# Kernel optimization log

Hardware: AMD Instinct MI355X
Metric: run time of the kernel (lower is better)

Reference implementation:

```python
import jax, jax.numpy as jnp
import numpy as np

BS, V, J = 256, 10475, 55
NSHAPE, NEXP = 300, 50

# SMPLX kinematic tree (fixed model constant)
PARENTS = np.array([
    -1, 0, 0, 0, 1, 2, 3, 4, 5, 6, 7, 8, 9, 9, 9, 12, 13, 14, 16, 17, 18, 19,
    15, 15, 15,
    20, 25, 26, 20, 28, 29, 20, 31, 32, 20, 34, 35, 20, 37, 38,
    21, 40, 41, 21, 43, 44, 21, 46, 47, 21, 49, 50, 21, 52, 53], dtype=np.int64)


def batch_rodrigues(rvec):
    # rvec: [N,3] axis-angle -> [N,3,3] rotation matrices
    angle = jnp.linalg.norm(rvec + 1e-8, axis=-1, keepdims=True)  # [N,1]
    axis = rvec / angle
    x, y, z = axis[..., 0], axis[..., 1], axis[..., 2]
    zr = jnp.zeros_like(x)
    K = jnp.stack([zr, -z, y, z, zr, -x, -y, x, zr], axis=-1).reshape(-1, 3, 3)
    s = jnp.sin(angle)[..., None]
    c = jnp.cos(angle)[..., None]
    I = jnp.eye(3, dtype=rvec.dtype)
    return I + s * K + (1.0 - c) * (K @ K)


def setup_inputs():
    key = jax.random.key(0)
    ks = jax.random.split(key, 9)
    pose = 0.2 * jax.random.normal(ks[0], (BS, 53, 3), jnp.float32)
    shape = jax.random.normal(ks[1], (BS, 10), jnp.float32)
    expression = jax.random.normal(ks[2], (BS, NEXP), jnp.float32)
    global_orient = 0.2 * jax.random.normal(ks[3], (1, 3), jnp.float32)
    v_template = jax.random.normal(ks[4], (V, 3), jnp.float32)
    shapedirs = 0.01 * jax.random.normal(ks[5], (V, 3, NSHAPE + NEXP), jnp.float32)
    posedirs = 0.01 * jax.random.normal(ks[6], (486, V * 3), jnp.float32)
    J_regressor = jax.random.uniform(ks[7], (J, V), jnp.float32)
    J_regressor = J_regressor / jnp.sum(J_regressor, axis=1, keepdims=True)
    lbs_weights = jax.random.uniform(ks[8], (V, J), jnp.float32)
    lbs_weights = lbs_weights / jnp.sum(lbs_weights, axis=1, keepdims=True)
    return {"pose": pose, "shape": shape, "expression": expression,
            "global_orient": global_orient, "v_template": v_template,
            "shapedirs": shapedirs, "posedirs": posedirs,
            "J_regressor": J_regressor, "lbs_weights": lbs_weights}


def lbs(betas, rot_mats, v_template, shapedirs, posedirs, J_regressor, lbs_weights):
    bs = betas.shape[0]
    dt = betas.dtype
    # shape blendshapes
    v_shaped = v_template[None] + jnp.einsum('bl,vcl->bvc', betas, shapedirs)
    # rest-pose joints
    joints = jnp.einsum('jv,bvc->bjc', J_regressor, v_shaped)  # [b,J,3]
    # pose blendshapes
    I3 = jnp.eye(3, dtype=dt)
    pose_feature = (rot_mats[:, 1:] - I3).reshape(bs, -1)  # [b,(J-1)*9]
    v_posed = v_shaped + jnp.einsum('bp,pn->bn', pose_feature, posedirs).reshape(bs, V, 3)
    # forward kinematics along the tree
    rel_joints = jnp.concatenate(
        [joints[:, :1], joints[:, 1:] - joints[:, PARENTS[1:]]], axis=1)
    top = jnp.concatenate([rot_mats, rel_joints[..., None]], axis=-1)  # [b,J,3,4]
    bot = jnp.broadcast_to(jnp.array([0, 0, 0, 1], dtype=dt), (bs, J, 1, 4))
    T_local = jnp.concatenate([top, bot], axis=-2)  # [b,J,4,4]
    A_list = [T_local[:, 0]]
    for j in range(1, J):  # fixed 55-joint chain
        A_list.append(A_list[int(PARENTS[j])] @ T_local[:, j])
    A = jnp.stack(A_list, axis=1)  # [b,J,4,4]
    posed_joints = A[..., :3, 3]
    # subtract rest-pose contribution
    corr = jnp.einsum('bjmn,bjn->bjm', A[..., :3, :3], joints)
    A_rel = A.at[..., :3, 3].add(-corr)
    # vertex skinning
    T = jnp.einsum('vj,bjmn->bvmn', lbs_weights, A_rel)  # [b,V,4,4]
    verts = jnp.einsum('bvmn,bvn->bvm', T[..., :3, :3], v_posed) + T[..., :3, 3]
    return verts, posed_joints


def reference(pose, shape, expression, global_orient, v_template, shapedirs,
              posedirs, J_regressor, lbs_weights):
    bs = pose.shape[0]
    dt = pose.dtype
    go = jnp.broadcast_to(global_orient[:, None, :], (bs, 1, 3))
    eyes = jnp.zeros((bs, 2, 3), dtype=dt)  # leye/reye fixed at zero
    # order: global, body(21), jaw, leye, reye, lhand(15), rhand(15) -> 55
    full_pose = jnp.concatenate(
        [go, pose[:, 1:22], pose[:, 52:53], eyes, pose[:, 22:37], pose[:, 37:52]],
        axis=1)
    betas = jnp.concatenate(
        [shape, jnp.zeros((bs, NSHAPE - shape.shape[1]), dtype=dt), expression],
        axis=1)  # [b,350]
    rot_mats = batch_rodrigues(full_pose.reshape(-1, 3)).reshape(bs, J, 3, 3)
    verts, joints = lbs(betas, rot_mats, v_template, shapedirs, posedirs,
                        J_regressor, lbs_weights)
    return verts, joints
```

## Files before the change

kernel.cpp:

```cpp
#include <hip/hip_runtime.h>
#include <math.h>

#define BS 256
#define V 10475
#define NJ 55
#define R3 31425
#define NP 486
#define LB 60
#define KP 576
#define VK 10496
#define JOFF 8044800
#define DSP 66

typedef __attribute__((ext_vector_type(8))) short short8;
typedef __attribute__((ext_vector_type(4))) float float4_;

__device__ const int PARENTS_d[NJ] = {
  -1, 0, 0, 0, 1, 2, 3, 4, 5, 6, 7, 8, 9, 9, 9, 12, 13, 14, 16, 17, 18, 19,
  15, 15, 15, 20, 25, 26, 20, 28, 29, 20, 31, 32, 20, 34, 35, 20, 37, 38,
  21, 40, 41, 21, 43, 44, 21, 46, 47, 21, 49, 50, 21, 52, 53
};

__device__ __forceinline__ unsigned short f2b(float f) {
  unsigned int u = __float_as_uint(f);
  unsigned int r = (u + 0x7FFFu + ((u >> 16) & 1u)) >> 16;
  return (unsigned short)r;
}

__global__ __launch_bounds__(256) void k_pose(
    const float* __restrict__ pose, const float* __restrict__ shp,
    const float* __restrict__ expr, const float* __restrict__ go,
    float* __restrict__ rot_ws, unsigned short* __restrict__ Ftr,
    float* __restrict__ betas_T) {
  int b = threadIdx.x;
  int j = blockIdx.x;
  if (j == NJ) {
    #pragma unroll
    for (int l = 0; l < 10; ++l) {
      float v = shp[b * 10 + l];
      betas_T[l * BS + b] = v;
      Ftr[(size_t)b * KP + NP + l] = f2b(v);
    }
    #pragma unroll
    for (int l = 0; l < 50; ++l) {
      float v = expr[b * 50 + l];
      betas_T[(10 + l) * BS + b] = v;
      Ftr[(size_t)b * KP + NP + 10 + l] = f2b(v);
    }
    #pragma unroll
    for (int l = NP + LB; l < KP; ++l) Ftr[(size_t)b * KP + l] = 0;
    return;
  }
  float rx, ry, rz;
  if (j == 0) { rx = go[0]; ry = go[1]; rz = go[2]; }
  else if (j == 23 || j == 24) { rx = 0.f; ry = 0.f; rz = 0.f; }
  else {
    int src = (j <= 21) ? j : (j == 22 ? 52 : j - 3);
    const float* p = pose + ((size_t)b * 53 + src) * 3;
    rx = p[0]; ry = p[1]; rz = p[2];
  }
  float sx = rx + 1e-8f, sy = ry + 1e-8f, sz = rz + 1e-8f;
  float ang = sqrtf(sx * sx + sy * sy + sz * sz);
  float inv = 1.f / ang;
  float x = rx * inv, y = ry * inv, z = rz * inv;
  float s = sinf(ang), c = cosf(ang), C = 1.f - c;
  float R[9];
  R[0] = 1.f - C * (y * y + z * z);
  R[1] = -s * z + C * x * y;
  R[2] =  s * y + C * x * z;
  R[3] =  s * z + C * x * y;
  R[4] = 1.f - C * (x * x + z * z);
  R[5] = -s * x + C * y * z;
  R[6] = -s * y + C * x * z;
  R[7] =  s * x + C * y * z;
  R[8] = 1.f - C * (x * x + y * y);
  float* rw = rot_ws + ((size_t)b * NJ + j) * 9;
  #pragma unroll
  for (int e = 0; e < 9; ++e) rw[e] = R[e];
  if (j >= 1) {
    int pb = (j - 1) * 9;
    #pragma unroll
    for (int e = 0; e < 9; ++e)
      Ftr[(size_t)b * KP + pb + e] =
          f2b(R[e] - ((e == 0 || e == 4 || e == 8) ? 1.f : 0.f));
  }
}

__global__ __launch_bounds__(256) void k_jregb(
    const float* __restrict__ Jreg, unsigned short* __restrict__ Jregb) {
  size_t idx = (size_t)blockIdx.x * 256 + threadIdx.x;
  int j = (int)(idx / VK);
  int v = (int)(idx - (size_t)j * VK);
  float val = (j < NJ && v < V) ? Jreg[(size_t)j * V + v] : 0.f;
  Jregb[idx] = f2b(val);
}

__global__ __launch_bounds__(256) void k_trX(
    const float* __restrict__ sd, const float* __restrict__ vt,
    unsigned short* __restrict__ XbT) {
  __shared__ float tile[192][65];
  int t = threadIdx.x;
  int v0 = blockIdx.x * 64;
  #pragma unroll 1
  for (int c = 0; c < 3; ++c) {
    for (int idx = t; idx < 3840; idx += 256) {
      int v_l = idx / 60, col = idx - v_l * 60;
      int v = v0 + v_l;
      int cidx = (col < 10) ? col : 290 + col;
      float val = (v < V) ? sd[((size_t)v * 3 + c) * 350 + cidx] : 0.f;
      tile[c * 64 + col][v_l] = val;
    }
  }
  for (int idx = t; idx < 768; idx += 256) {
    int v_l = idx & 63, rr = idx >> 6;
    int c = rr >> 2, l = 60 + (rr & 3);
    int v = v0 + v_l;
    float val = (l == 60 && v < V) ? vt[(size_t)v * 3 + c] : 0.f;
    tile[c * 64 + l][v_l] = val;
  }
  __syncthreads();
  for (int idx = t; idx < 192 * 64; idx += 256) {
    int cl = idx >> 6, v_l = idx & 63;
    XbT[(size_t)cl * VK + v0 + v_l] = f2b(tile[cl][v_l]);
  }
}

__global__ __launch_bounds__(256) void k_jsm(
    const unsigned short* __restrict__ Jregb,
    const unsigned short* __restrict__ XbT, float* __restrict__ JS) {
  int lane = threadIdx.x & 63;
  int wv = threadIdx.x >> 6;
  int l15 = lane & 15, q = lane >> 4;
  int k0 = blockIdx.x * 128;
  const unsigned short* ap = Jregb + (size_t)(wv * 16 + l15) * VK + k0 + q * 8;
  float4_ acc[12];
  #pragma unroll
  for (int nt = 0; nt < 12; ++nt) acc[nt] = (float4_)0.f;
  #pragma unroll
  for (int ks = 0; ks < 4; ++ks) {
    short8 a = *(const short8*)(ap + ks * 32);
    #pragma unroll
    for (int nt = 0; nt < 12; ++nt) {
      const unsigned short* bp =
          XbT + (size_t)(nt * 16 + l15) * VK + k0 + ks * 32 + q * 8;
      short8 b = *(const short8*)bp;
      acc[nt] = __builtin_amdgcn_mfma_f32_16x16x32_bf16(a, b, acc[nt], 0, 0, 0);
    }
  }
  #pragma unroll
  for (int nt = 0; nt < 12; ++nt) {
    int cl = nt * 16 + l15;
    int c = cl >> 6, l = cl & 63;
    if (l < 61) {
      #pragma unroll
      for (int reg = 0; reg < 4; ++reg) {
        int jj = wv * 16 + q * 4 + reg;
        if (jj < NJ)
          atomicAdd(&JS[((size_t)jj * 3 + c) * 61 + l], acc[nt][reg]);
      }
    }
  }
}

__global__ __launch_bounds__(256) void k_wb(
    const float* __restrict__ lbs, unsigned short* __restrict__ Wb) {
  int v0 = blockIdx.x * 16;
  for (int idx = threadIdx.x; idx < 1024; idx += 256) {
    int v_l = idx >> 6, k = idx & 63;
    int v = v0 + v_l;
    float val = (k < NJ && v < V) ? lbs[(size_t)v * NJ + k] : 0.f;
    if (v < VK) Wb[(size_t)v * 64 + k] = f2b(val);
  }
}

__global__ __launch_bounds__(64) void k_chain(
    const float* __restrict__ JS, const float* __restrict__ betas_T,
    const float* __restrict__ rot_ws, unsigned short* __restrict__ arelb,
    float* __restrict__ out) {
  int b = blockIdx.x;
  int lane = threadIdx.x;
  __shared__ float joints_l[165];
  __shared__ float Tl[880];
  __shared__ float A[880];
  for (int idx = lane; idx < 165; idx += 64) {
    float sacc = JS[idx * 61 + 60];
    #pragma unroll
    for (int l = 0; l < LB; ++l) sacc += JS[idx * 61 + l] * betas_T[l * BS + b];
    joints_l[idx] = sacc;
  }
  __syncthreads();
  for (int idx = lane; idx < 880; idx += 64) {
    int j = idx >> 4, e = idx & 15, r = e >> 2, cc = e & 3;
    float val;
    if (r < 3) {
      if (cc < 3) val = rot_ws[((size_t)b * NJ + j) * 9 + r * 3 + cc];
      else {
        int par = PARENTS_d[j];
        val = joints_l[j * 3 + r] - (par >= 0 ? joints_l[par * 3 + r] : 0.f);
      }
    } else val = (cc == 3) ? 1.f : 0.f;
    Tl[idx] = val;
  }
  __syncthreads();
  if (lane < 16) A[lane] = Tl[lane];
  __syncthreads();
  for (int j = 1; j < NJ; ++j) {
    int par = PARENTS_d[j];
    if (lane < 16) {
      int r = lane >> 2, cc = lane & 3;
      float sacc = 0.f;
      #pragma unroll
      for (int k = 0; k < 4; ++k)
        sacc += A[par * 16 + r * 4 + k] * Tl[j * 16 + k * 4 + cc];
      A[j * 16 + lane] = sacc;
    }
    __syncthreads();
  }
  for (int idx = lane; idx < 165; idx += 64) {
    int j = idx / 3, r = idx % 3;
    out[JOFF + (size_t)b * 165 + idx] = A[j * 16 + r * 4 + 3];
  }
  for (int idx = lane; idx < 1024; idx += 64) {
    int n = idx >> 6, k = idx & 63;
    float val = 0.f;
    if (n < 12 && k < NJ) {
      int m = n >> 2, cc = n & 3;
      if (cc < 3) val = A[k * 16 + m * 4 + cc];
      else {
        val = A[k * 16 + m * 4 + 3]
            - (A[k * 16 + m * 4 + 0] * joints_l[k * 3 + 0] +
               A[k * 16 + m * 4 + 1] * joints_l[k * 3 + 1] +
               A[k * 16 + m * 4 + 2] * joints_l[k * 3 + 2]);
      }
    }
    arelb[(size_t)b * 1024 + idx] = f2b(val);
  }
}

__global__ __launch_bounds__(256) void k_gemm(
    const float* __restrict__ vt, const float* __restrict__ sd,
    const float* __restrict__ pd, const unsigned short* __restrict__ Ftr,
    float* __restrict__ out) {
  __shared__ float dsb[2][32 * DSP];
  int t = threadIdx.x;
  int lane = t & 63, wv = t >> 6;
  int l15 = lane & 15, q = lane >> 4;
  int r0 = blockIdx.x * 64;
  int m0 = wv * 64;
  int k_l = t >> 3;
  int c8 = (t & 7) * 8;
  bool full = (r0 + 64 <= R3);

  float4_ acc[4][4];
  #pragma unroll
  for (int mt = 0; mt < 4; ++mt)
    #pragma unroll
    for (int nt = 0; nt < 4; ++nt) acc[mt][nt] = (float4_)0.f;

  const unsigned short* aBase[4];
  #pragma unroll
  for (int mt = 0; mt < 4; ++mt)
    aBase[mt] = Ftr + (size_t)(m0 + mt * 16 + l15) * KP + q * 8;

  {
    int kg = k_l;
    float* dp = &dsb[0][k_l * DSP + c8];
    if (full) {
      const float* p = pd + (size_t)kg * R3 + r0 + c8;
      #pragma unroll
      for (int i = 0; i < 8; ++i) dp[i] = p[i];
    } else {
      #pragma unroll
      for (int i = 0; i < 8; ++i) {
        int r = r0 + c8 + i;
        dp[i] = (r < R3) ? pd[(size_t)kg * R3 + r] : 0.f;
      }
    }
  }
  __syncthreads();

  #pragma unroll 1
  for (int c = 0; c < 18; ++c) {
    int cur = c & 1;
    float sv[8];
    if (c < 17) {
      int kg = (c + 1) * 32 + k_l;
      if (kg < NP) {
        if (full) {
          const float* p = pd + (size_t)kg * R3 + r0 + c8;
          #pragma unroll
          for (int i = 0; i < 8; ++i) sv[i] = p[i];
        } else {
          #pragma unroll
          for (int i = 0; i < 8; ++i) {
            int r = r0 + c8 + i;
            sv[i] = (r < R3) ? pd[(size_t)kg * R3 + r] : 0.f;
          }
        }
      } else if (kg < NP + LB) {
        int ll = kg - NP;
        int cidx = (ll < 10) ? ll : (290 + ll);
        #pragma unroll
        for (int i = 0; i < 8; ++i) {
          int r = r0 + c8 + i;
          sv[i] = (r < R3) ? sd[(size_t)r * 350 + cidx] : 0.f;
        }
      } else {
        #pragma unroll
        for (int i = 0; i < 8; ++i) sv[i] = 0.f;
      }
    }
    short8 bf[4];
    #pragma unroll
    for (int nt = 0; nt < 4; ++nt) {
      unsigned short h[8];
      #pragma unroll
      for (int i = 0; i < 8; ++i)
        h[i] = f2b(dsb[cur][(q * 8 + i) * DSP + nt * 16 + l15]);
      short8 v;
      #pragma unroll
      for (int i = 0; i < 8; ++i) v[i] = (short)h[i];
      bf[nt] = v;
    }
    short8 af[4];
    #pragma unroll
    for (int mt = 0; mt < 4; ++mt)
      af[mt] = *(const short8*)(aBase[mt] + c * 32);
    #pragma unroll
    for (int mt = 0; mt < 4; ++mt)
      #pragma unroll
      for (int nt = 0; nt < 4; ++nt)
        acc[mt][nt] = __builtin_amdgcn_mfma_f32_16x16x32_bf16(
            af[mt], bf[nt], acc[mt][nt], 0, 0, 0);
    if (c < 17) {
      float* dp = &dsb[cur ^ 1][k_l * DSP + c8];
      #pragma unroll
      for (int i = 0; i < 8; ++i) dp[i] = sv[i];
    }
    __syncthreads();
  }

  #pragma unroll
  for (int nt = 0; nt < 4; ++nt) {
    int r = r0 + nt * 16 + l15;
    if (r < R3) {
      float vtv = vt[r];
      #pragma unroll
      for (int mt = 0; mt < 4; ++mt) {
        int bb = m0 + mt * 16 + q * 4;
        #pragma unroll
        for (int reg = 0; reg < 4; ++reg)
          out[(size_t)(bb + reg) * R3 + r] = acc[mt][nt][reg] + vtv;
      }
    }
  }
}

__global__ __launch_bounds__(256) void k_skin(
    const unsigned short* __restrict__ Wb, const unsigned short* __restrict__ arelb,
    float* __restrict__ out) {
  int lane = threadIdx.x & 63;
  int wv = threadIdx.x >> 6;
  int l15 = lane & 15, q = lane >> 4;
  int v = blockIdx.x * 64 + wv * 16 + l15;
  bool vok = (v < V);
  int b0 = blockIdx.y * 16;

  const unsigned short* wp = Wb + (size_t)v * 64 + q * 8;
  short8 w0 = *(const short8*)(wp);
  short8 w1 = *(const short8*)(wp + 32);

  const unsigned short* ap = arelb + (size_t)b0 * 1024 + l15 * 64 + q * 8;
  short8 a0 = *(const short8*)ap;
  short8 a1 = *(const short8*)(ap + 32);

  #pragma unroll 1
  for (int bi = 0; bi < 16; ++bi) {
    int b = b0 + bi;
    float* vp = out + (size_t)b * R3 + v * 3;
    float x = 0.f, y = 0.f, z = 0.f;
    if (vok && q < 3) { x = vp[0]; y = vp[1]; z = vp[2]; }
    short8 na0 = a0, na1 = a1;
    if (bi < 15) {
      const unsigned short* np = arelb + (size_t)(b + 1) * 1024 + l15 * 64 + q * 8;
      na0 = *(const short8*)np;
      na1 = *(const short8*)(np + 32);
    }
    float4_ acc = (float4_)0.f;
    acc = __builtin_amdgcn_mfma_f32_16x16x32_bf16(a0, w0, acc, 0, 0, 0);
    acc = __builtin_amdgcn_mfma_f32_16x16x32_bf16(a1, w1, acc, 0, 0, 0);
    if (vok && q < 3)
      vp[q] = acc[0] * x + acc[1] * y + acc[2] * z + acc[3];
    a0 = na0; a1 = na1;
  }
}

extern "C" void kernel_launch(void* const* d_in, const int* in_sizes, int n_in,
                              void* d_out, int out_size, void* d_ws, size_t ws_size,
                              hipStream_t stream) {
  const float* pose = (const float*)d_in[0];
  const float* shp  = (const float*)d_in[1];
  const float* expr = (const float*)d_in[2];
  const float* go   = (const float*)d_in[3];
  const float* vt   = (const float*)d_in[4];
  const float* sd   = (const float*)d_in[5];
  const float* pd   = (const float*)d_in[6];
  const float* jr   = (const float*)d_in[7];
  const float* lbs  = (const float*)d_in[8];
  float* out = (float*)d_out;
  float* ws  = (float*)d_ws;

  float* betas_T        = ws;
  float* rot_ws         = ws + 15360;
  float* JS             = ws + 142080;
  unsigned short* Ftr   = (unsigned short*)(ws + 152160);
  unsigned short* arelb = (unsigned short*)(ws + 225888);
  unsigned short* Wb    = (unsigned short*)(ws + 356960);
  unsigned short* Jregb = (unsigned short*)(ws + 692832);
  unsigned short* XbT   = (unsigned short*)(ws + 1028704);

  hipMemsetAsync(JS, 0, 10080 * sizeof(float), stream);
  k_pose<<<NJ + 1, 256, 0, stream>>>(pose, shp, expr, go, rot_ws, Ftr, betas_T);
  k_jregb<<<(64 * VK) / 256, 256, 0, stream>>>(jr, Jregb);
  k_trX<<<VK / 64, 256, 0, stream>>>(sd, vt, XbT);
  k_jsm<<<VK / 128, 256, 0, stream>>>(Jregb, XbT, JS);
  k_wb<<<VK / 16, 256, 0, stream>>>(lbs, Wb);
  k_chain<<<BS, 64, 0, stream>>>(JS, betas_T, rot_ws, arelb, out);
  k_gemm<<<492, 256, 0, stream>>>(vt, sd, pd, Ftr, out);
  k_skin<<<dim3(164, 16), 256, 0, stream>>>(Wb, arelb, out);
}
```

Measured before the change: 311.4 us.

## Pack bf16 pairs in shared memory, coalesce skin loads, split jsm finer

In the pose GEMM, the posedirs tile is converted to bf16 when it is stored to shared memory, two K rows packed per 32-bit word. This removes the per-element float-to-bf16 conversion and strided LDS reads from the MFMA operand build. The skinning kernel now has each lane read and write contiguous vertex coordinates, moving the transform entries and xyz values between lanes with shuffles so global accesses coalesce. The joint-regressor kernel also uses half-size K slices over twice as many blocks, which means more atomic partial sums.

```diff
diff --git a/kernel.cpp b/kernel.cpp
--- a/kernel.cpp
+++ b/kernel.cpp
@@ -10,10 +10,11 @@
 #define KP 576
 #define VK 10496
 #define JOFF 8044800
-#define DSP 66
+#define PR 65
 
 typedef __attribute__((ext_vector_type(8))) short short8;
 typedef __attribute__((ext_vector_type(4))) float float4_;
+typedef __attribute__((ext_vector_type(4))) unsigned int uint4_;
 
 __device__ const int PARENTS_d[NJ] = {
   -1, 0, 0, 0, 1, 2, 3, 4, 5, 6, 7, 8, 9, 9, 9, 12, 13, 14, 16, 17, 18, 19,
@@ -131,13 +132,13 @@
   int lane = threadIdx.x & 63;
   int wv = threadIdx.x >> 6;
   int l15 = lane & 15, q = lane >> 4;
-  int k0 = blockIdx.x * 128;
+  int k0 = blockIdx.x * 64;
   const unsigned short* ap = Jregb + (size_t)(wv * 16 + l15) * VK + k0 + q * 8;
   float4_ acc[12];
   #pragma unroll
   for (int nt = 0; nt < 12; ++nt) acc[nt] = (float4_)0.f;
   #pragma unroll
-  for (int ks = 0; ks < 4; ++ks) {
+  for (int ks = 0; ks < 2; ++ks) {
     short8 a = *(const short8*)(ap + ks * 32);
     #pragma unroll
     for (int nt = 0; nt < 12; ++nt) {
@@ -241,14 +242,14 @@
     const float* __restrict__ vt, const float* __restrict__ sd,
     const float* __restrict__ pd, const unsigned short* __restrict__ Ftr,
     float* __restrict__ out) {
-  __shared__ float dsb[2][32 * DSP];
+  __shared__ unsigned int pk[2][16 * PR];
   int t = threadIdx.x;
-  int lane = t & 63, wv = t >> 6;
+  int lane = t & 63, wvv = t >> 6;
   int l15 = lane & 15, q = lane >> 4;
   int r0 = blockIdx.x * 64;
-  int m0 = wv * 64;
-  int k_l = t >> 3;
-  int c8 = (t & 7) * 8;
+  int m0 = wvv * 64;
+  int kp_ = t >> 4;
+  int c4 = (t & 15) * 4;
   bool full = (r0 + 64 <= R3);
 
   float4_ acc[4][4];
@@ -263,64 +264,64 @@
     aBase[mt] = Ftr + (size_t)(m0 + mt * 16 + l15) * KP + q * 8;
 
   {
-    int kg = k_l;
-    float* dp = &dsb[0][k_l * DSP + c8];
-    if (full) {
-      const float* p = pd + (size_t)kg * R3 + r0 + c8;
-      #pragma unroll
-      for (int i = 0; i < 8; ++i) dp[i] = p[i];
-    } else {
-      #pragma unroll
-      for (int i = 0; i < 8; ++i) {
-        int r = r0 + c8 + i;
-        dp[i] = (r < R3) ? pd[(size_t)kg * R3 + r] : 0.f;
-      }
-    }
+    float v0[4], v1[4];
+    int kg = kp_ * 2;
+    #pragma unroll
+    for (int i = 0; i < 4; ++i) {
+      int r = r0 + c4 + i;
+      bool ok = full || (r < R3);
+      v0[i] = ok ? pd[(size_t)kg * R3 + r] : 0.f;
+      v1[i] = ok ? pd[(size_t)(kg + 1) * R3 + r] : 0.f;
+    }
+    #pragma unroll
+    for (int i = 0; i < 4; ++i)
+      pk[0][kp_ * PR + c4 + i] =
+          (unsigned)f2b(v0[i]) | ((unsigned)f2b(v1[i]) << 16);
   }
   __syncthreads();
 
   #pragma unroll 1
   for (int c = 0; c < 18; ++c) {
     int cur = c & 1;
-    float sv[8];
+    unsigned int dnext[4];
     if (c < 17) {
-      int kg = (c + 1) * 32 + k_l;
-      if (kg < NP) {
-        if (full) {
-          const float* p = pd + (size_t)kg * R3 + r0 + c8;
+      float v0[4], v1[4];
+      int kg = (c + 1) * 32 + kp_ * 2;
+      #pragma unroll
+      for (int h = 0; h < 2; ++h) {
+        int k = kg + h;
+        float* dst = h ? v1 : v0;
+        if (k < NP) {
           #pragma unroll
-          for (int i = 0; i < 8; ++i) sv[i] = p[i];
+          for (int i = 0; i < 4; ++i) {
+            int r = r0 + c4 + i;
+            dst[i] = (full || r < R3) ? pd[(size_t)k * R3 + r] : 0.f;
+          }
+        } else if (k < NP + LB) {
+          int ll = k - NP;
+          int cidx = (ll < 10) ? ll : (290 + ll);
+          #pragma unroll
+          for (int i = 0; i < 4; ++i) {
+            int r = r0 + c4 + i;
+            dst[i] = (r < R3) ? sd[(size_t)r * 350 + cidx] : 0.f;
+          }
         } else {
           #pragma unroll
-          for (int i = 0; i < 8; ++i) {
-            int r = r0 + c8 + i;
-            sv[i] = (r < R3) ? pd[(size_t)kg * R3 + r] : 0.f;
-          }
+          for (int i = 0; i < 4; ++i) dst[i] = 0.f;
         }
-      } else if (kg < NP + LB) {
-        int ll = kg - NP;
-        int cidx = (ll < 10) ? ll : (290 + ll);
-        #pragma unroll
-        for (int i = 0; i < 8; ++i) {
-          int r = r0 + c8 + i;
-          sv[i] = (r < R3) ? sd[(size_t)r * 350 + cidx] : 0.f;
-        }
-      } else {
-        #pragma unroll
-        for (int i = 0; i < 8; ++i) sv[i] = 0.f;
       }
+      #pragma unroll
+      for (int i = 0; i < 4; ++i)
+        dnext[i] = (unsigned)f2b(v0[i]) | ((unsigned)f2b(v1[i]) << 16);
     }
     short8 bf[4];
     #pragma unroll
     for (int nt = 0; nt < 4; ++nt) {
-      unsigned short h[8];
-      #pragma unroll
-      for (int i = 0; i < 8; ++i)
-        h[i] = f2b(dsb[cur][(q * 8 + i) * DSP + nt * 16 + l15]);
-      short8 v;
-      #pragma unroll
-      for (int i = 0; i < 8; ++i) v[i] = (short)h[i];
-      bf[nt] = v;
+      uint4_ u;
+      #pragma unroll
+      for (int jd = 0; jd < 4; ++jd)
+        u[jd] = pk[cur][(q * 4 + jd) * PR + nt * 16 + l15];
+      bf[nt] = __builtin_bit_cast(short8, u);
     }
     short8 af[4];
     #pragma unroll
@@ -333,9 +334,9 @@
         acc[mt][nt] = __builtin_amdgcn_mfma_f32_16x16x32_bf16(
             af[mt], bf[nt], acc[mt][nt], 0, 0, 0);
     if (c < 17) {
-      float* dp = &dsb[cur ^ 1][k_l * DSP + c8];
-      #pragma unroll
-      for (int i = 0; i < 8; ++i) dp[i] = sv[i];
+      #pragma unroll
+      for (int i = 0; i < 4; ++i)
+        pk[cur ^ 1][kp_ * PR + c4 + i] = dnext[i];
     }
     __syncthreads();
   }
@@ -362,14 +363,24 @@
   int lane = threadIdx.x & 63;
   int wv = threadIdx.x >> 6;
   int l15 = lane & 15, q = lane >> 4;
-  int v = blockIdx.x * 64 + wv * 16 + l15;
-  bool vok = (v < V);
+  int v0w = blockIdx.x * 64 + wv * 16;
   int b0 = blockIdx.y * 16;
 
-  const unsigned short* wp = Wb + (size_t)v * 64 + q * 8;
+  const unsigned short* wp = Wb + (size_t)(v0w + l15) * 64 + q * 8;
   short8 w0 = *(const short8*)(wp);
   short8 w1 = *(const short8*)(wp + 32);
 
+  int vi = lane / 3 >= 16 ? 15 : lane / 3;
+  vi = lane / 3;
+  int ci = lane - vi * 3;
+  int srcT = ci * 16 + (vi & 15);
+  int srcX = (vi & 15) * 3 + ((vi >> 4) * 48);
+  srcX = vi * 3 <= 63 ? vi * 3 : 63;
+  int r = v0w * 3 + lane;
+  bool rok = (lane < 48) && (r < R3);
+
+  float vload = 0.f;
+  if (rok) vload = out[(size_t)b0 * R3 + r];
   const unsigned short* ap = arelb + (size_t)b0 * 1024 + l15 * 64 + q * 8;
   short8 a0 = *(const short8*)ap;
   short8 a1 = *(const short8*)(ap + 32);
@@ -377,11 +388,10 @@
   #pragma unroll 1
   for (int bi = 0; bi < 16; ++bi) {
     int b = b0 + bi;
-    float* vp = out + (size_t)b * R3 + v * 3;
-    float x = 0.f, y = 0.f, z = 0.f;
-    if (vok && q < 3) { x = vp[0]; y = vp[1]; z = vp[2]; }
+    float nvload = 0.f;
     short8 na0 = a0, na1 = a1;
     if (bi < 15) {
+      if (rok) nvload = out[(size_t)(b + 1) * R3 + r];
       const unsigned short* np = arelb + (size_t)(b + 1) * 1024 + l15 * 64 + q * 8;
       na0 = *(const short8*)np;
       na1 = *(const short8*)(np + 32);
@@ -389,9 +399,15 @@
     float4_ acc = (float4_)0.f;
     acc = __builtin_amdgcn_mfma_f32_16x16x32_bf16(a0, w0, acc, 0, 0, 0);
     acc = __builtin_amdgcn_mfma_f32_16x16x32_bf16(a1, w1, acc, 0, 0, 0);
-    if (vok && q < 3)
-      vp[q] = acc[0] * x + acc[1] * y + acc[2] * z + acc[3];
-    a0 = na0; a1 = na1;
+    float T0 = __shfl(acc[0], srcT, 64);
+    float T1 = __shfl(acc[1], srcT, 64);
+    float T2 = __shfl(acc[2], srcT, 64);
+    float T3 = __shfl(acc[3], srcT, 64);
+    float x = __shfl(vload, srcX, 64);
+    float y = __shfl(vload, srcX + 1 <= 63 ? srcX + 1 : 63, 64);
+    float z = __shfl(vload, srcX + 2 <= 63 ? srcX + 2 : 63, 64);
+    if (rok) out[(size_t)b * R3 + r] = T0 * x + T1 * y + T2 * z + T3;
+    vload = nvload; a0 = na0; a1 = na1;
   }
 }
 
@@ -423,7 +439,7 @@
   k_pose<<<NJ + 1, 256, 0, stream>>>(pose, shp, expr, go, rot_ws, Ftr, betas_T);
   k_jregb<<<(64 * VK) / 256, 256, 0, stream>>>(jr, Jregb);
   k_trX<<<VK / 64, 256, 0, stream>>>(sd, vt, XbT);
-  k_jsm<<<VK / 128, 256, 0, stream>>>(Jregb, XbT, JS);
+  k_jsm<<<VK / 64, 256, 0, stream>>>(Jregb, XbT, JS);
   k_wb<<<VK / 16, 256, 0, stream>>>(lbs, Wb);
   k_chain<<<BS, 64, 0, stream>>>(JS, betas_T, rot_ws, arelb, out);
   k_gemm<<<492, 256, 0, stream>>>(vt, sd, pd, Ftr, out);
```

After: 327.8 us. 1.05x slower.
